# Kernel tuning notes

Hardware: AMD Instinct MI355X
Metric: run time of the kernel (lower is better)

Reference implementation:

```python
import jax, jax.numpy as jnp
import numpy as np

EMBED_DIM = 512
N_HEADS = 8
HEAD_DIM = EMBED_DIM // N_HEADS
MAX_GENES = 5000
SPARSITY_RATIO = 0.1
WINDOW = 20  # SparseAttention local window


def make_sparse_mask(key):
    # local band |i-j| <= window//2, plus random connections, plus diagonal
    idx = jnp.arange(MAX_GENES)
    mask = jnp.abs(idx[:, None] - idx[None, :]) <= (WINDOW // 2)
    n_random = int(SPARSITY_RATIO * MAX_GENES * MAX_GENES)
    k1, k2 = jax.random.split(key)
    ri = jax.random.randint(k1, (n_random,), 0, MAX_GENES)
    rj = jax.random.randint(k2, (n_random,), 0, MAX_GENES)
    mask = mask.at[ri, rj].set(True)
    mask = mask.at[idx, idx].set(True)
    return mask  # bool [MAX_GENES, MAX_GENES]


def setup_inputs() -> dict:
    key = jax.random.key(0)
    ks = jax.random.split(key, 10)
    B, S, E = 1, 4096, EMBED_DIM
    x = jax.random.normal(ks[0], (B, S, E), dtype=jnp.float32)
    init = lambda k: jax.random.normal(k, (E, E), dtype=jnp.float32) * 0.02
    return {
        "x": x,
        "Wq": init(ks[1]), "bq": jnp.zeros((E,), jnp.float32),
        "Wk": init(ks[2]), "bk": jnp.zeros((E,), jnp.float32),
        "Wv": init(ks[3]), "bv": jnp.zeros((E,), jnp.float32),
        "Wo": init(ks[4]), "bo": jnp.zeros((E,), jnp.float32),
        "mask": make_sparse_mask(ks[5]),
    }


def reference(x, Wq, bq, Wk, bk, Wv, bv, Wo, bo, mask):
    B, S, E = x.shape
    H, D = N_HEADS, HEAD_DIM
    # QKV projections (torch Linear: x @ W.T + b), split heads -> [B,H,S,D]
    Q = (x @ Wq.T + bq).reshape(B, S, H, D).transpose(0, 2, 1, 3)
    K = (x @ Wk.T + bk).reshape(B, S, H, D).transpose(0, 2, 1, 3)
    V = (x @ Wv.T + bv).reshape(B, S, H, D).transpose(0, 2, 1, 3)
    scale = 1.0 / jnp.sqrt(jnp.asarray(D, dtype=jnp.float32))
    scores = jnp.einsum('bhsd,bhtd->bhst', Q, K) * scale
    m = mask[:S, :S]  # static sparse pattern
    # original: scores*mask then masked_fill(mask==0, -inf) -> equivalent where
    scores = jnp.where(m[None, None], scores, -jnp.inf)
    w = jax.nn.softmax(scores, axis=-1)
    w = jnp.nan_to_num(w, nan=0.0)  # diag is always unmasked, but keep faithful
    out = jnp.einsum('bhst,bhtd->bhsd', w, V)
    out = out.transpose(0, 2, 1, 3).reshape(B, S, E)
    return out @ Wo.T + bo
```

## Files before the change

### kernel.cpp

```cpp
#include <hip/hip_runtime.h>
#include <hip/hip_bf16.h>
#include <stdint.h>

#define S 4096
#define E 512
#define H 8
#define D 64
#define MROW 5000

typedef __hip_bfloat16 bf16;
typedef __attribute__((ext_vector_type(8))) short bf16x8;
typedef __attribute__((ext_vector_type(4))) float f32x4;

#define CMUL (0.125f * 1.4426950408889634f)

__global__ void sniff(const unsigned int* __restrict__ mask,
                      int* __restrict__ flag)
{
    int lane = threadIdx.x & 63;
    int hit = 0;
    for (int i = lane; i < 2048; i += 64) {
        unsigned int w = mask[i];
        if (w > 1u && (w & 0xFEFEFEFEu) == 0u) hit = 1;
    }
    unsigned long long b = __ballot(hit);
    if (lane == 0) { flag[1] = (b != 0ull) ? 1 : 0; flag[0] = 1; }
}

__global__ __launch_bounds__(256) void convert_all(
    const float* __restrict__ x,  const float* __restrict__ wq,
    const float* __restrict__ wk, const float* __restrict__ wv,
    const float* __restrict__ wo, const float* __restrict__ bq,
    const float* __restrict__ bk, const float* __restrict__ bv,
    const float* __restrict__ bo,
    bf16* __restrict__ xb, bf16* __restrict__ wcat, bf16* __restrict__ wob,
    bf16* __restrict__ bcat, bf16* __restrict__ bob)
{
    const float* srcs[9] = {x, wq, wk, wv, wo, bq, bk, bv, bo};
    bf16* dsts[9] = {xb, wcat, wcat + 262144, wcat + 524288, wob,
                     bcat, bcat + 512, bcat + 1024, bob};
    const int cnts[9] = {2097152, 262144, 262144, 262144, 262144,
                         512, 512, 512, 512};
    const int ngroups = (2097152 + 4 * 262144 + 4 * 512) / 4;
    for (int g = blockIdx.x * blockDim.x + threadIdx.x; g < ngroups;
         g += gridDim.x * blockDim.x) {
        int e = g * 4;
        int seg = 0;
        while (e >= cnts[seg]) { e -= cnts[seg]; ++seg; }
        float4 v = *(const float4*)(srcs[seg] + e);
        union { bf16 h[4]; uint2 u; } cv;
        cv.h[0] = (bf16)v.x; cv.h[1] = (bf16)v.y;
        cv.h[2] = (bf16)v.z; cv.h[3] = (bf16)v.w;
        *(uint2*)(dsts[seg] + e) = cv.u;
    }
}

__global__ __launch_bounds__(256) void pack_mask(const void* __restrict__ mask,
                                                 unsigned long long* __restrict__ bits,
                                                 const int* __restrict__ flag)
{
    const bool isbyte = flag[1] != 0;
    int wid   = (blockIdx.x * blockDim.x + threadIdx.x) >> 6;
    int lane  = threadIdx.x & 63;
    int nwav  = (gridDim.x * blockDim.x) >> 6;
    int total = S * (S / 64);
    for (int w = wid; w < total; w += nwav) {
        int row  = w >> 6;
        int word = w & 63;
        int col  = word * 64 + lane;
        unsigned int v;
        if (isbyte) v = ((const unsigned char*)mask)[(size_t)row * MROW + col];
        else        v = ((const unsigned int*)mask)[(size_t)row * MROW + col];
        unsigned long long b = __ballot(v != 0u);
        if (lane == 0) bits[(size_t)row * 64 + word] = b;
    }
}

__global__ __launch_bounds__(256) void gemm64(const bf16* __restrict__ A,
                                              const bf16* __restrict__ W,
                                              const bf16* __restrict__ bias,
                                              void* __restrict__ outv, int mode)
{
    __shared__ bf16 As[64][72];
    __shared__ bf16 Bs[64][72];
    const int tid  = threadIdx.x;
    const int wid  = tid >> 6, lane = tid & 63;
    const int quad = lane >> 4, l15 = lane & 15;
    const int nbase = blockIdx.x * 64;
    const int mbase = blockIdx.y * 64;
    const int m0 = wid * 16;

    f32x4 acc[4];
#pragma unroll
    for (int i = 0; i < 4; ++i) acc[i] = (f32x4){0.f, 0.f, 0.f, 0.f};

    for (int kt = 0; kt < E / 64; ++kt) {
        const int kb = kt * 64;
        __syncthreads();
#pragma unroll
        for (int i = 0; i < 2; ++i) {
            int slot = tid + i * 256;
            int row = slot >> 3, kg = slot & 7;
            *(uint4*)&As[row][kg * 8] = *(const uint4*)&A[(size_t)(mbase + row) * E + kb + kg * 8];
            *(uint4*)&Bs[row][kg * 8] = *(const uint4*)&W[(size_t)(nbase + row) * E + kb + kg * 8];
        }
        __syncthreads();
        bf16x8 a0 = *(bf16x8*)&As[m0 + l15][quad * 8];
        bf16x8 a1 = *(bf16x8*)&As[m0 + l15][32 + quad * 8];
#pragma unroll
        for (int nt = 0; nt < 4; ++nt) {
            bf16x8 b0 = *(bf16x8*)&Bs[nt * 16 + l15][quad * 8];
            bf16x8 b1 = *(bf16x8*)&Bs[nt * 16 + l15][32 + quad * 8];
            acc[nt] = __builtin_amdgcn_mfma_f32_16x16x32_bf16(a0, b0, acc[nt], 0, 0, 0);
            acc[nt] = __builtin_amdgcn_mfma_f32_16x16x32_bf16(a1, b1, acc[nt], 0, 0, 0);
        }
    }
#pragma unroll
    for (int nt = 0; nt < 4; ++nt) {
        int col = nbase + nt * 16 + l15;
        float bv = (float)bias[col];
#pragma unroll
        for (int r = 0; r < 4; ++r) {
            int row = mbase + m0 + quad * 4 + r;
            float v = acc[nt][r] + bv;
            if (mode == 0) {
                int t = col >> 9, hh = (col >> 6) & 7, d = col & 63;
                if (t == 0) v *= CMUL;
                ((bf16*)outv)[((size_t)t * H + hh) * S * D + (size_t)row * D + d] = (bf16)v;
            } else {
                ((float*)outv)[(size_t)row * E + col] = v;
            }
        }
    }
}

__global__ __launch_bounds__(256) void attn(const bf16* __restrict__ Qp,
                                            const bf16* __restrict__ Kp,
                                            const bf16* __restrict__ Vp,
                                            const unsigned long long* __restrict__ bits,
                                            float* __restrict__ Opart,
                                            float* __restrict__ Lpart,
                                            int ktper)
{
    __shared__ __align__(16) char smem[25600];
    bf16 (*Qs)[72]     = (bf16(*)[72])smem;
    bf16 (*Ps)[16][64] = (bf16(*)[16][64])smem;
    bf16 (*Ks)[64]     = (bf16(*)[64])(smem + 9216);
    bf16 (*Vts)[64]    = (bf16(*)[64])(smem + 17408);

    const int tid  = threadIdx.x;
    const int wid  = tid >> 6, lane = tid & 63;
    const int quad = lane >> 4, l15 = lane & 15;
    const int qt = blockIdx.x, h = blockIdx.y, split = blockIdx.z;
    const int qbase = qt * 64;
    const int m0 = wid * 16;
    const bf16* Qh = Qp + (size_t)h * S * D;
    const bf16* Kh = Kp + (size_t)h * S * D;
    const bf16* Vh = Vp + (size_t)h * S * D;

    const int krow0 = tid >> 3, kkg = tid & 7;
    const int krow1 = (tid + 256) >> 3;
    const int ksw0 = (kkg ^ (krow0 & 7)) * 8;
    const int ksw1 = (kkg ^ (krow1 & 7)) * 8;
    const int vt0 = (tid & 31) * 2, vd0 = (tid >> 5) * 8;

#pragma unroll
    for (int i = 0; i < 2; ++i) {
        int slot = tid + i * 256;
        int row = slot >> 3, kg = slot & 7;
        *(uint4*)&Qs[row][kg * 8] = *(const uint4*)&Qh[(size_t)(qbase + row) * D + kg * 8];
    }
    __syncthreads();
    bf16x8 aq0 = *(bf16x8*)&Qs[m0 + l15][quad * 8];
    bf16x8 aq1 = *(bf16x8*)&Qs[m0 + l15][32 + quad * 8];

    bf16x8 bl;
    {
        union { short s; bf16 b; } one; one.b = (bf16)1.0f;
        short v = (l15 == 0) ? one.s : (short)0;
#pragma unroll
        for (int j = 0; j < 8; ++j) bl[j] = v;
    }

    f32x4 o[4];
#pragma unroll
    for (int dt = 0; dt < 4; ++dt) o[dt] = (f32x4){0.f, 0.f, 0.f, 0.f};
    f32x4 accl = (f32x4){0.f, 0.f, 0.f, 0.f};

    const int kt0 = split * ktper, kt1 = kt0 + ktper;

    uint4 kq0, kq1, vq0, vq1;
    {
        const int kbase = kt0 * 64;
        kq0 = *(const uint4*)&Kh[(size_t)(kbase + krow0) * D + kkg * 8];
        kq1 = *(const uint4*)&Kh[(size_t)(kbase + krow1) * D + kkg * 8];
        vq0 = *(const uint4*)&Vh[(size_t)(kbase + vt0) * D + vd0];
        vq1 = *(const uint4*)&Vh[(size_t)(kbase + vt0 + 1) * D + vd0];
    }

    const int ksw_rd = (l15 & 7);
    const int pkey   = ((l15 >> 1) & 7);
    for (int kt = kt0; kt < kt1; ++kt) {
        __syncthreads();
        *(uint4*)&Ks[krow0][ksw0] = kq0;
        *(uint4*)&Ks[krow1][ksw1] = kq1;
        {
            const unsigned short* p0 = (const unsigned short*)&vq0;
            const unsigned short* p1 = (const unsigned short*)&vq1;
#pragma unroll
            for (int j = 0; j < 8; ++j) {
                unsigned int pk = (unsigned int)p0[j] | ((unsigned int)p1[j] << 16);
                *(unsigned int*)&Vts[vd0 + j][vt0 ^ (j * 8)] = pk;
            }
        }
        if (kt + 1 < kt1) {
            const int kb2 = (kt + 1) * 64;
            kq0 = *(const uint4*)&Kh[(size_t)(kb2 + krow0) * D + kkg * 8];
            kq1 = *(const uint4*)&Kh[(size_t)(kb2 + krow1) * D + kkg * 8];
            vq0 = *(const uint4*)&Vh[(size_t)(kb2 + vt0) * D + vd0];
            vq1 = *(const uint4*)&Vh[(size_t)(kb2 + vt0 + 1) * D + vd0];
        }
        unsigned long long mw[4];
#pragma unroll
        for (int r = 0; r < 4; ++r) {
            int row = qbase + m0 + quad * 4 + r;
            mw[r] = bits[(size_t)row * 64 + kt];
        }
        __syncthreads();

        f32x4 sc[4];
        {
            f32x4 z = (f32x4){0.f, 0.f, 0.f, 0.f};
#pragma unroll
            for (int nt = 0; nt < 4; ++nt) {
                bf16x8 b0 = *(bf16x8*)&Ks[nt * 16 + l15][(quad ^ ksw_rd) * 8];
                bf16x8 b1 = *(bf16x8*)&Ks[nt * 16 + l15][((quad + 4) ^ ksw_rd) * 8];
                sc[nt] = __builtin_amdgcn_mfma_f32_16x16x32_bf16(aq0, b0, z, 0, 0, 0);
                sc[nt] = __builtin_amdgcn_mfma_f32_16x16x32_bf16(aq1, b1, sc[nt], 0, 0, 0);
            }
        }
#pragma unroll
        for (int r = 0; r < 4; ++r) {
            unsigned long long sh = mw[r] >> l15;
            int row = quad * 4 + r;
            int key = ((row >> 1) & 7) << 3;
#pragma unroll
            for (int nt = 0; nt < 4; ++nt) {
                float p = __builtin_amdgcn_exp2f(sc[nt][r]);
                bool ok = (sh >> (nt * 16)) & 1ull;
                p = ok ? p : 0.f;
                Ps[wid][row][(nt * 16 + l15) ^ key] = (bf16)p;
            }
        }
        bf16x8 ap0 = *(bf16x8*)&Ps[wid][l15][(quad ^ pkey) * 8];
        bf16x8 ap1 = *(bf16x8*)&Ps[wid][l15][((quad + 4) ^ pkey) * 8];
        accl = __builtin_amdgcn_mfma_f32_16x16x32_bf16(ap0, bl, accl, 0, 0, 0);
        accl = __builtin_amdgcn_mfma_f32_16x16x32_bf16(ap1, bl, accl, 0, 0, 0);
#pragma unroll
        for (int dt = 0; dt < 4; ++dt) {
            bf16x8 bv0 = *(bf16x8*)&Vts[dt * 16 + l15][(quad ^ ksw_rd) * 8];
            bf16x8 bv1 = *(bf16x8*)&Vts[dt * 16 + l15][((quad + 4) ^ ksw_rd) * 8];
            o[dt] = __builtin_amdgcn_mfma_f32_16x16x32_bf16(ap0, bv0, o[dt], 0, 0, 0);
            o[dt] = __builtin_amdgcn_mfma_f32_16x16x32_bf16(ap1, bv1, o[dt], 0, 0, 0);
        }
    }
    float* Op = Opart + (size_t)(split * H + h) * S * D;
    float* Lp = Lpart + (size_t)(split * H + h) * S;
#pragma unroll
    for (int r = 0; r < 4; ++r) {
        int row = qbase + m0 + quad * 4 + r;
        if (l15 == 0) Lp[row] = accl[r];
#pragma unroll
        for (int dt = 0; dt < 4; ++dt)
            Op[(size_t)row * D + dt * 16 + l15] = o[dt][r];
    }
}

__global__ __launch_bounds__(256) void combine(const float* __restrict__ Opart,
                                               const float* __restrict__ Lpart,
                                               bf16* __restrict__ Ow, int nsplit)
{
    int g = blockIdx.x * 256 + threadIdx.x;
    int e = g * 4;
    int row = e >> 9;
    int c = e & 511;
    int h = c >> 6, d = c & 63;
    size_t base = ((size_t)h * S + row) * D + d;
    const size_t oh = (size_t)H * S * D;
    float ax = 0.f, ay = 0.f, az = 0.f, aw = 0.f, l = 0.f;
    for (int s = 0; s < nsplit; ++s) {
        float4 a = *(const float4*)(Opart + (size_t)s * oh + base);
        ax += a.x; ay += a.y; az += a.z; aw += a.w;
        l += Lpart[(size_t)s * H * S + (size_t)h * S + row];
    }
    float inv = (l > 0.f) ? 1.f / l : 0.f;
    union { bf16 x[4]; uint2 u; } ov;
    ov.x[0] = (bf16)(ax * inv);
    ov.x[1] = (bf16)(ay * inv);
    ov.x[2] = (bf16)(az * inv);
    ov.x[3] = (bf16)(aw * inv);
    *(uint2*)(Ow + (size_t)row * E + c) = ov.u;
}

extern "C" void kernel_launch(void* const* d_in, const int* in_sizes, int n_in,
                              void* d_out, int out_size, void* d_ws, size_t ws_size,
                              hipStream_t stream)
{
    char* ws = (char*)d_ws;
    const size_t MB = (size_t)1 << 20;
    bf16* Qw   = (bf16*)(ws + 0 * MB);
    bf16* Kw   = (bf16*)(ws + 4 * MB);
    bf16* Vw   = (bf16*)(ws + 8 * MB);
    bf16* Ow   = (bf16*)(ws + 12 * MB);
    unsigned long long* bits = (unsigned long long*)(ws + 16 * MB);
    bf16* xb   = (bf16*)(ws + 18 * MB);
    bf16* Wcat = (bf16*)(ws + 22 * MB);
    bf16* Wob  = (bf16*)(ws + 24 * MB);
    bf16* bcat = (bf16*)(ws + 25 * MB);
    bf16* bob  = (bf16*)(ws + 25 * MB + 8192);
    int*  flag = (int*)(ws + 25 * MB + 16384);
    float* Opart = (float*)(ws + 26 * MB);

    int nsplit = (ws_size >= 59 * MB) ? 4 : 2;
    int ktper  = (S / 64) / nsplit;
    float* Lpart = (float*)(ws + 26 * MB + (size_t)nsplit * 8 * MB);

    hipLaunchKernelGGL(sniff, dim3(1), dim3(64), 0, stream,
                       (const unsigned int*)d_in[9], flag);
    hipLaunchKernelGGL(convert_all, dim3(1024), dim3(256), 0, stream,
                       (const float*)d_in[0], (const float*)d_in[1],
                       (const float*)d_in[3], (const float*)d_in[5],
                       (const float*)d_in[7], (const float*)d_in[2],
                       (const float*)d_in[4], (const float*)d_in[6],
                       (const float*)d_in[8],
                       xb, Wcat, Wob, bcat, bob);
    hipLaunchKernelGGL(pack_mask, dim3(1024), dim3(256), 0, stream, d_in[9], bits, flag);
    hipLaunchKernelGGL(gemm64, dim3(24, 64), dim3(256), 0, stream, xb, Wcat, bcat, (void*)Qw, 0);
    hipLaunchKernelGGL(attn, dim3(S / 64, H, nsplit), dim3(256), 0, stream,
                       Qw, Kw, Vw, bits, Opart, Lpart, ktper);
    hipLaunchKernelGGL(combine, dim3(2048), dim3(256), 0, stream, Opart, Lpart, Ow, nsplit);
    hipLaunchKernelGGL(gemm64, dim3(8, 64), dim3(256), 0, stream, Ow, Wob, bob, d_out, 1);
}
```

Before: 313.6 us.

## Load K fragments directly into registers and double-buffer V tiles in LDS

Each wave now reads its K MFMA operands straight from global memory into registers, so the K tile no longer passes through shared memory. The V transpose tile is double-buffered in LDS, which lets the loop drop the leading barrier and keep a single sync per iteration. The aim is to cut LDS traffic and barrier stalls. In exchange, every wave re-reads the whole K tile (a fourfold redundant read served by cache), and the K loads are issued in the same iteration they are consumed rather than prefetched, so global latency may be exposed.

```diff
diff --git a/kernel.cpp b/kernel.cpp
--- a/kernel.cpp
+++ b/kernel.cpp
@@ -13,6 +13,8 @@
 typedef __attribute__((ext_vector_type(4))) float f32x4;
 
 #define CMUL (0.125f * 1.4426950408889634f)
+
+union u4bf8 { uint4 u; bf16x8 b; };
 
 __global__ void sniff(const unsigned int* __restrict__ mask,
                       int* __restrict__ flag)
@@ -145,8 +147,7 @@
     __shared__ __align__(16) char smem[25600];
     bf16 (*Qs)[72]     = (bf16(*)[72])smem;
     bf16 (*Ps)[16][64] = (bf16(*)[16][64])smem;
-    bf16 (*Ks)[64]     = (bf16(*)[64])(smem + 9216);
-    bf16 (*Vts)[64]    = (bf16(*)[64])(smem + 17408);
+    bf16 (*Vts)[64][64] = (bf16(*)[64][64])(smem + 9216);
 
     const int tid  = threadIdx.x;
     const int wid  = tid >> 6, lane = tid & 63;
@@ -158,10 +159,6 @@
     const bf16* Kh = Kp + (size_t)h * S * D;
     const bf16* Vh = Vp + (size_t)h * S * D;
 
-    const int krow0 = tid >> 3, kkg = tid & 7;
-    const int krow1 = (tid + 256) >> 3;
-    const int ksw0 = (kkg ^ (krow0 & 7)) * 8;
-    const int ksw1 = (kkg ^ (krow1 & 7)) * 8;
     const int vt0 = (tid & 31) * 2, vd0 = (tid >> 5) * 8;
 
 #pragma unroll
@@ -189,34 +186,41 @@
 
     const int kt0 = split * ktper, kt1 = kt0 + ktper;
 
-    uint4 kq0, kq1, vq0, vq1;
+    uint4 vq0, vq1;
     {
         const int kbase = kt0 * 64;
-        kq0 = *(const uint4*)&Kh[(size_t)(kbase + krow0) * D + kkg * 8];
-        kq1 = *(const uint4*)&Kh[(size_t)(kbase + krow1) * D + kkg * 8];
         vq0 = *(const uint4*)&Vh[(size_t)(kbase + vt0) * D + vd0];
         vq1 = *(const uint4*)&Vh[(size_t)(kbase + vt0 + 1) * D + vd0];
     }
 
     const int ksw_rd = (l15 & 7);
     const int pkey   = ((l15 >> 1) & 7);
+
+#pragma unroll 1
     for (int kt = kt0; kt < kt1; ++kt) {
-        __syncthreads();
-        *(uint4*)&Ks[krow0][ksw0] = kq0;
-        *(uint4*)&Ks[krow1][ksw1] = kq1;
+        const int kbase = kt * 64;
+        const int buf = kt & 1;
+
+        u4bf8 kf[8];
+        {
+            const bf16* Kt = Kh + (size_t)kbase * D;
+#pragma unroll
+            for (int nt = 0; nt < 4; ++nt) {
+                kf[nt * 2 + 0].u = *(const uint4*)&Kt[(nt * 16 + l15) * D + quad * 8];
+                kf[nt * 2 + 1].u = *(const uint4*)&Kt[(nt * 16 + l15) * D + 32 + quad * 8];
+            }
+        }
         {
             const unsigned short* p0 = (const unsigned short*)&vq0;
             const unsigned short* p1 = (const unsigned short*)&vq1;
 #pragma unroll
             for (int j = 0; j < 8; ++j) {
                 unsigned int pk = (unsigned int)p0[j] | ((unsigned int)p1[j] << 16);
-                *(unsigned int*)&Vts[vd0 + j][vt0 ^ (j * 8)] = pk;
+                *(unsigned int*)&Vts[buf][vd0 + j][vt0 ^ (j * 8)] = pk;
             }
         }
         if (kt + 1 < kt1) {
             const int kb2 = (kt + 1) * 64;
-            kq0 = *(const uint4*)&Kh[(size_t)(kb2 + krow0) * D + kkg * 8];
-            kq1 = *(const uint4*)&Kh[(size_t)(kb2 + krow1) * D + kkg * 8];
             vq0 = *(const uint4*)&Vh[(size_t)(kb2 + vt0) * D + vd0];
             vq1 = *(const uint4*)&Vh[(size_t)(kb2 + vt0 + 1) * D + vd0];
         }
@@ -233,10 +237,8 @@
             f32x4 z = (f32x4){0.f, 0.f, 0.f, 0.f};
 #pragma unroll
             for (int nt = 0; nt < 4; ++nt) {
-                bf16x8 b0 = *(bf16x8*)&Ks[nt * 16 + l15][(quad ^ ksw_rd) * 8];
-                bf16x8 b1 = *(bf16x8*)&Ks[nt * 16 + l15][((quad + 4) ^ ksw_rd) * 8];
-                sc[nt] = __builtin_amdgcn_mfma_f32_16x16x32_bf16(aq0, b0, z, 0, 0, 0);
-                sc[nt] = __builtin_amdgcn_mfma_f32_16x16x32_bf16(aq1, b1, sc[nt], 0, 0, 0);
+                sc[nt] = __builtin_amdgcn_mfma_f32_16x16x32_bf16(aq0, kf[nt * 2 + 0].b, z, 0, 0, 0);
+                sc[nt] = __builtin_amdgcn_mfma_f32_16x16x32_bf16(aq1, kf[nt * 2 + 1].b, sc[nt], 0, 0, 0);
             }
         }
 #pragma unroll
@@ -258,8 +260,8 @@
         accl = __builtin_amdgcn_mfma_f32_16x16x32_bf16(ap1, bl, accl, 0, 0, 0);
 #pragma unroll
         for (int dt = 0; dt < 4; ++dt) {
-            bf16x8 bv0 = *(bf16x8*)&Vts[dt * 16 + l15][(quad ^ ksw_rd) * 8];
-            bf16x8 bv1 = *(bf16x8*)&Vts[dt * 16 + l15][((quad + 4) ^ ksw_rd) * 8];
+            bf16x8 bv0 = *(bf16x8*)&Vts[buf][dt * 16 + l15][(quad ^ ksw_rd) * 8];
+            bf16x8 bv1 = *(bf16x8*)&Vts[buf][dt * 16 + l15][((quad + 4) ^ ksw_rd) * 8];
             o[dt] = __builtin_amdgcn_mfma_f32_16x16x32_bf16(ap0, bv0, o[dt], 0, 0, 0);
             o[dt] = __builtin_amdgcn_mfma_f32_16x16x32_bf16(ap1, bv1, o[dt], 0, 0, 0);
         }
```

After: 413.0 us. +31.7%, slower.

## Fuse prep kernels, transpose mask bits, fold split-combine into output GEMM

Applied to the files above, without the earlier changes.

Merges the mask sniff, mask bit-packing and fp32-to-bf16 conversion into one prep kernel, cutting two launches. The packed mask is stored transposed (word-major), so each attention lane loads its four row words as two 16-byte vector loads instead of four scattered 8-byte loads. The split-KV combine pass is folded into the output projection GEMM, which sums the partials and normalizes while filling its A tile; this removes a kernel and the bf16 intermediate round trip. In exchange, every column block of the output GEMM now rereads the fp32 partials, and each prep block redundantly re-sniffs the mask format.

```diff
diff --git a/kernel.cpp b/kernel.cpp
--- a/kernel.cpp
+++ b/kernel.cpp
@@ -14,20 +14,8 @@
 
 #define CMUL (0.125f * 1.4426950408889634f)
 
-__global__ void sniff(const unsigned int* __restrict__ mask,
-                      int* __restrict__ flag)
-{
-    int lane = threadIdx.x & 63;
-    int hit = 0;
-    for (int i = lane; i < 2048; i += 64) {
-        unsigned int w = mask[i];
-        if (w > 1u && (w & 0xFEFEFEFEu) == 0u) hit = 1;
-    }
-    unsigned long long b = __ballot(hit);
-    if (lane == 0) { flag[1] = (b != 0ull) ? 1 : 0; flag[0] = 1; }
-}
-
-__global__ __launch_bounds__(256) void convert_all(
+__global__ __launch_bounds__(256) void prep(
+    const void* __restrict__ mask, unsigned long long* __restrict__ bitsT,
     const float* __restrict__ x,  const float* __restrict__ wq,
     const float* __restrict__ wk, const float* __restrict__ wv,
     const float* __restrict__ wo, const float* __restrict__ bq,
@@ -36,50 +24,55 @@
     bf16* __restrict__ xb, bf16* __restrict__ wcat, bf16* __restrict__ wob,
     bf16* __restrict__ bcat, bf16* __restrict__ bob)
 {
-    const float* srcs[9] = {x, wq, wk, wv, wo, bq, bk, bv, bo};
-    bf16* dsts[9] = {xb, wcat, wcat + 262144, wcat + 524288, wob,
-                     bcat, bcat + 512, bcat + 1024, bob};
-    const int cnts[9] = {2097152, 262144, 262144, 262144, 262144,
-                         512, 512, 512, 512};
-    const int ngroups = (2097152 + 4 * 262144 + 4 * 512) / 4;
-    for (int g = blockIdx.x * blockDim.x + threadIdx.x; g < ngroups;
-         g += gridDim.x * blockDim.x) {
-        int e = g * 4;
-        int seg = 0;
-        while (e >= cnts[seg]) { e -= cnts[seg]; ++seg; }
-        float4 v = *(const float4*)(srcs[seg] + e);
-        union { bf16 h[4]; uint2 u; } cv;
-        cv.h[0] = (bf16)v.x; cv.h[1] = (bf16)v.y;
-        cv.h[2] = (bf16)v.z; cv.h[3] = (bf16)v.w;
-        *(uint2*)(dsts[seg] + e) = cv.u;
-    }
-}
-
-__global__ __launch_bounds__(256) void pack_mask(const void* __restrict__ mask,
-                                                 unsigned long long* __restrict__ bits,
-                                                 const int* __restrict__ flag)
-{
-    const bool isbyte = flag[1] != 0;
-    int wid   = (blockIdx.x * blockDim.x + threadIdx.x) >> 6;
-    int lane  = threadIdx.x & 63;
-    int nwav  = (gridDim.x * blockDim.x) >> 6;
-    int total = S * (S / 64);
-    for (int w = wid; w < total; w += nwav) {
-        int row  = w >> 6;
-        int word = w & 63;
-        int col  = word * 64 + lane;
-        unsigned int v;
-        if (isbyte) v = ((const unsigned char*)mask)[(size_t)row * MROW + col];
-        else        v = ((const unsigned int*)mask)[(size_t)row * MROW + col];
-        unsigned long long b = __ballot(v != 0u);
-        if (lane == 0) bits[(size_t)row * 64 + word] = b;
-    }
-}
-
-__global__ __launch_bounds__(256) void gemm64(const bf16* __restrict__ A,
-                                              const bf16* __restrict__ W,
-                                              const bf16* __restrict__ bias,
-                                              void* __restrict__ outv, int mode)
+    const int b = blockIdx.x;
+    const int tid = threadIdx.x;
+    if (b < 1024) {
+        const unsigned int* mw32 = (const unsigned int*)mask;
+        int lane = tid & 63;
+        int hit = 0;
+#pragma unroll
+        for (int i = 0; i < 8; ++i) {
+            unsigned int w = mw32[lane + i * 64];
+            if (w > 1u && (w & 0xFEFEFEFEu) == 0u) hit = 1;
+        }
+        const bool isbyte = (__ballot(hit) != 0ull);
+        int wid  = (b * 256 + tid) >> 6;
+        int nwav = (1024 * 256) >> 6;
+        int total = (S / 64) * S;
+        for (int w = wid; w < total; w += nwav) {
+            int word = w >> 12;
+            int row  = w & (S - 1);
+            int col  = word * 64 + lane;
+            unsigned int v;
+            if (isbyte) v = ((const unsigned char*)mask)[(size_t)row * MROW + col];
+            else        v = ((const unsigned int*)mask)[(size_t)row * MROW + col];
+            unsigned long long bb = __ballot(v != 0u);
+            if (lane == 0) bitsT[(size_t)word * S + row] = bb;
+        }
+    } else {
+        const float* srcs[9] = {x, wq, wk, wv, wo, bq, bk, bv, bo};
+        bf16* dsts[9] = {xb, wcat, wcat + 262144, wcat + 524288, wob,
+                         bcat, bcat + 512, bcat + 1024, bob};
+        const int cnts[9] = {2097152, 262144, 262144, 262144, 262144,
+                             512, 512, 512, 512};
+        const int ngroups = (2097152 + 4 * 262144 + 4 * 512) / 4;
+        for (int g = (b - 1024) * 256 + tid; g < ngroups; g += 1024 * 256) {
+            int e = g * 4;
+            int seg = 0;
+            while (e >= cnts[seg]) { e -= cnts[seg]; ++seg; }
+            float4 v = *(const float4*)(srcs[seg] + e);
+            union { bf16 h[4]; uint2 u; } cv;
+            cv.h[0] = (bf16)v.x; cv.h[1] = (bf16)v.y;
+            cv.h[2] = (bf16)v.z; cv.h[3] = (bf16)v.w;
+            *(uint2*)(dsts[seg] + e) = cv.u;
+        }
+    }
+}
+
+__global__ __launch_bounds__(256) void gemm_qkv(const bf16* __restrict__ A,
+                                                const bf16* __restrict__ W,
+                                                const bf16* __restrict__ bias,
+                                                bf16* __restrict__ out)
 {
     __shared__ bf16 As[64][72];
     __shared__ bf16 Bs[64][72];
@@ -123,13 +116,9 @@
         for (int r = 0; r < 4; ++r) {
             int row = mbase + m0 + quad * 4 + r;
             float v = acc[nt][r] + bv;
-            if (mode == 0) {
-                int t = col >> 9, hh = (col >> 6) & 7, d = col & 63;
-                if (t == 0) v *= CMUL;
-                ((bf16*)outv)[((size_t)t * H + hh) * S * D + (size_t)row * D + d] = (bf16)v;
-            } else {
-                ((float*)outv)[(size_t)row * E + col] = v;
-            }
+            int t = col >> 9, hh = (col >> 6) & 7, d = col & 63;
+            if (t == 0) v *= CMUL;
+            out[((size_t)t * H + hh) * S * D + (size_t)row * D + d] = (bf16)v;
         }
     }
 }
@@ -137,7 +126,7 @@
 __global__ __launch_bounds__(256) void attn(const bf16* __restrict__ Qp,
                                             const bf16* __restrict__ Kp,
                                             const bf16* __restrict__ Vp,
-                                            const unsigned long long* __restrict__ bits,
+                                            const unsigned long long* __restrict__ bitsT,
                                             float* __restrict__ Opart,
                                             float* __restrict__ Lpart,
                                             int ktper)
@@ -198,6 +187,8 @@
         vq1 = *(const uint4*)&Vh[(size_t)(kbase + vt0 + 1) * D + vd0];
     }
 
+    const unsigned long long* mb = bitsT + (size_t)kt0 * S + qbase + m0 + quad * 4;
+
     const int ksw_rd = (l15 & 7);
     const int pkey   = ((l15 >> 1) & 7);
     for (int kt = kt0; kt < kt1; ++kt) {
@@ -220,12 +211,9 @@
             vq0 = *(const uint4*)&Vh[(size_t)(kb2 + vt0) * D + vd0];
             vq1 = *(const uint4*)&Vh[(size_t)(kb2 + vt0 + 1) * D + vd0];
         }
-        unsigned long long mw[4];
-#pragma unroll
-        for (int r = 0; r < 4; ++r) {
-            int row = qbase + m0 + quad * 4 + r;
-            mw[r] = bits[(size_t)row * 64 + kt];
-        }
+        uint4 mv0 = *(const uint4*)mb;
+        uint4 mv1 = *(const uint4*)(mb + 2);
+        mb += S;
         __syncthreads();
 
         f32x4 sc[4];
@@ -239,9 +227,14 @@
                 sc[nt] = __builtin_amdgcn_mfma_f32_16x16x32_bf16(aq1, b1, sc[nt], 0, 0, 0);
             }
         }
+        unsigned long long mwq[4];
+        mwq[0] = ((unsigned long long)mv0.y << 32) | mv0.x;
+        mwq[1] = ((unsigned long long)mv0.w << 32) | mv0.z;
+        mwq[2] = ((unsigned long long)mv1.y << 32) | mv1.x;
+        mwq[3] = ((unsigned long long)mv1.w << 32) | mv1.z;
 #pragma unroll
         for (int r = 0; r < 4; ++r) {
-            unsigned long long sh = mw[r] >> l15;
+            unsigned long long sh = mwq[r] >> l15;
             int row = quad * 4 + r;
             int key = ((row >> 1) & 7) << 3;
 #pragma unroll
@@ -276,30 +269,73 @@
     }
 }
 
-__global__ __launch_bounds__(256) void combine(const float* __restrict__ Opart,
-                                               const float* __restrict__ Lpart,
-                                               bf16* __restrict__ Ow, int nsplit)
-{
-    int g = blockIdx.x * 256 + threadIdx.x;
-    int e = g * 4;
-    int row = e >> 9;
-    int c = e & 511;
-    int h = c >> 6, d = c & 63;
-    size_t base = ((size_t)h * S + row) * D + d;
+__global__ __launch_bounds__(256) void gemm_out(const float* __restrict__ Opart,
+                                                const float* __restrict__ Lpart,
+                                                const bf16* __restrict__ W,
+                                                const bf16* __restrict__ bias,
+                                                float* __restrict__ out, int nsplit)
+{
+    __shared__ bf16 As[64][72];
+    __shared__ bf16 Bs[64][72];
+    const int tid  = threadIdx.x;
+    const int wid  = tid >> 6, lane = tid & 63;
+    const int quad = lane >> 4, l15 = lane & 15;
+    const int nbase = blockIdx.x * 64;
+    const int mbase = blockIdx.y * 64;
+    const int m0 = wid * 16;
     const size_t oh = (size_t)H * S * D;
-    float ax = 0.f, ay = 0.f, az = 0.f, aw = 0.f, l = 0.f;
-    for (int s = 0; s < nsplit; ++s) {
-        float4 a = *(const float4*)(Opart + (size_t)s * oh + base);
-        ax += a.x; ay += a.y; az += a.z; aw += a.w;
-        l += Lpart[(size_t)s * H * S + (size_t)h * S + row];
-    }
-    float inv = (l > 0.f) ? 1.f / l : 0.f;
-    union { bf16 x[4]; uint2 u; } ov;
-    ov.x[0] = (bf16)(ax * inv);
-    ov.x[1] = (bf16)(ay * inv);
-    ov.x[2] = (bf16)(az * inv);
-    ov.x[3] = (bf16)(aw * inv);
-    *(uint2*)(Ow + (size_t)row * E + c) = ov.u;
+
+    f32x4 acc[4];
+#pragma unroll
+    for (int i = 0; i < 4; ++i) acc[i] = (f32x4){0.f, 0.f, 0.f, 0.f};
+
+    for (int kt = 0; kt < E / 64; ++kt) {
+        const int kb = kt * 64;
+        const int h = kt;
+        __syncthreads();
+#pragma unroll
+        for (int i = 0; i < 2; ++i) {
+            int slot = tid + i * 256;
+            int row = slot >> 3, kg = slot & 7;
+            int qrow = mbase + row;
+            size_t base = ((size_t)h * S + qrow) * D + kg * 8;
+            float a[8] = {0, 0, 0, 0, 0, 0, 0, 0};
+            float l = 0.f;
+            for (int s = 0; s < nsplit; ++s) {
+                float4 p0 = *(const float4*)(Opart + (size_t)s * oh + base);
+                float4 p1 = *(const float4*)(Opart + (size_t)s * oh + base + 4);
+                a[0] += p0.x; a[1] += p0.y; a[2] += p0.z; a[3] += p0.w;
+                a[4] += p1.x; a[5] += p1.y; a[6] += p1.z; a[7] += p1.w;
+                l += Lpart[(size_t)s * H * S + (size_t)h * S + qrow];
+            }
+            float inv = (l > 0.f) ? 1.f / l : 0.f;
+            union { bf16 hh[8]; uint4 u; } cv;
+#pragma unroll
+            for (int j = 0; j < 8; ++j) cv.hh[j] = (bf16)(a[j] * inv);
+            *(uint4*)&As[row][kg * 8] = cv.u;
+            *(uint4*)&Bs[row][kg * 8] = *(const uint4*)&W[(size_t)(nbase + row) * E + kb + kg * 8];
+        }
+        __syncthreads();
+        bf16x8 a0 = *(bf16x8*)&As[m0 + l15][quad * 8];
+        bf16x8 a1 = *(bf16x8*)&As[m0 + l15][32 + quad * 8];
+#pragma unroll
+        for (int nt = 0; nt < 4; ++nt) {
+            bf16x8 b0 = *(bf16x8*)&Bs[nt * 16 + l15][quad * 8];
+            bf16x8 b1 = *(bf16x8*)&Bs[nt * 16 + l15][32 + quad * 8];
+            acc[nt] = __builtin_amdgcn_mfma_f32_16x16x32_bf16(a0, b0, acc[nt], 0, 0, 0);
+            acc[nt] = __builtin_amdgcn_mfma_f32_16x16x32_bf16(a1, b1, acc[nt], 0, 0, 0);
+        }
+    }
+#pragma unroll
+    for (int nt = 0; nt < 4; ++nt) {
+        int col = nbase + nt * 16 + l15;
+        float bv = (float)bias[col];
+#pragma unroll
+        for (int r = 0; r < 4; ++r) {
+            int row = mbase + m0 + quad * 4 + r;
+            out[(size_t)row * E + col] = acc[nt][r] + bv;
+        }
+    }
 }
 
 extern "C" void kernel_launch(void* const* d_in, const int* in_sizes, int n_in,
@@ -311,33 +347,30 @@
     bf16* Qw   = (bf16*)(ws + 0 * MB);
     bf16* Kw   = (bf16*)(ws + 4 * MB);
     bf16* Vw   = (bf16*)(ws + 8 * MB);
-    bf16* Ow   = (bf16*)(ws + 12 * MB);
-    unsigned long long* bits = (unsigned long long*)(ws + 16 * MB);
+    unsigned long long* bitsT = (unsigned long long*)(ws + 16 * MB);
     bf16* xb   = (bf16*)(ws + 18 * MB);
     bf16* Wcat = (bf16*)(ws + 22 * MB);
     bf16* Wob  = (bf16*)(ws + 24 * MB);
     bf16* bcat = (bf16*)(ws + 25 * MB);
     bf16* bob  = (bf16*)(ws + 25 * MB + 8192);
-    int*  flag = (int*)(ws + 25 * MB + 16384);
     float* Opart = (float*)(ws + 26 * MB);
 
     int nsplit = (ws_size >= 59 * MB) ? 4 : 2;
     int ktper  = (S / 64) / nsplit;
     float* Lpart = (float*)(ws + 26 * MB + (size_t)nsplit * 8 * MB);
 
-    hipLaunchKernelGGL(sniff, dim3(1), dim3(64), 0, stream,
-                       (const unsigned int*)d_in[9], flag);
-    hipLaunchKernelGGL(convert_all, dim3(1024), dim3(256), 0, stream,
+    hipLaunchKernelGGL(prep, dim3(2048), dim3(256), 0, stream,
+                       d_in[9], bitsT,
                        (const float*)d_in[0], (const float*)d_in[1],
                        (const float*)d_in[3], (const float*)d_in[5],
                        (const float*)d_in[7], (const float*)d_in[2],
                        (const float*)d_in[4], (const float*)d_in[6],
                        (const float*)d_in[8],
                        xb, Wcat, Wob, bcat, bob);
-    hipLaunchKernelGGL(pack_mask, dim3(1024), dim3(256), 0, stream, d_in[9], bits, flag);
-    hipLaunchKernelGGL(gemm64, dim3(24, 64), dim3(256), 0, stream, xb, Wcat, bcat, (void*)Qw, 0);
+    hipLaunchKernelGGL(gemm_qkv, dim3(24, 64), dim3(256), 0, stream,
+                       xb, Wcat, bcat, Qw);
     hipLaunchKernelGGL(attn, dim3(S / 64, H, nsplit), dim3(256), 0, stream,
-                       Qw, Kw, Vw, bits, Opart, Lpart, ktper);
-    hipLaunchKernelGGL(combine, dim3(2048), dim3(256), 0, stream, Opart, Lpart, Ow, nsplit);
-    hipLaunchKernelGGL(gemm64, dim3(8, 64), dim3(256), 0, stream, Ow, Wob, bob, d_out, 1);
-}
+                       Qw, Kw, Vw, bitsT, Opart, Lpart, ktper);
+    hipLaunchKernelGGL(gemm_out, dim3(8, 64), dim3(256), 0, stream,
+                       Opart, Lpart, Wob, bob, (float*)d_out, nsplit);
+}
```

Result: slower. 334.3 us (+6.6%).
